# Performance work log

Hardware: AMD Instinct MI355X
Metric: run time of the kernel (lower is better)

Reference implementation:

```python
import jax, jax.numpy as jnp
import numpy as np

N_NODES = 65536
N_PER = 1024      # nodes per graph
NUM_GRAPHS = 64
N_EDGES = 1048576
IN_DIM = 192
PE_DIM = 64
HIDDEN = 256
LATENT = 128
POOL_RATIO = 0.5
K_PER = int(np.ceil(POOL_RATIO * N_PER))  # 512 kept per graph


def setup_inputs() -> dict:
    key = jax.random.key(0)
    ks = jax.random.split(key, 12)
    x_raw = jax.random.normal(ks[0], (N_NODES, IN_DIM), dtype=jnp.float32)
    sincos_pe = jax.random.normal(ks[1], (N_NODES, PE_DIM), dtype=jnp.float32)
    edge_index = jax.random.randint(ks[2], (2, N_EDGES), 0, N_NODES, dtype=jnp.int64)
    batch = (jnp.arange(N_NODES, dtype=jnp.int64) // N_PER)
    eps = jax.random.normal(ks[3], (N_NODES, LATENT), dtype=jnp.float32)
    # learned parameters (GCNConv: Linear no-bias weight + separate bias; TopKPooling weight)
    def glorot(k, shape):
        lim = float(np.sqrt(6.0 / (shape[0] + shape[1])))
        return jax.random.uniform(k, shape, jnp.float32, -lim, lim)
    W1 = glorot(ks[4], (IN_DIM + PE_DIM, HIDDEN))
    b1 = jnp.zeros((HIDDEN,), jnp.float32)
    Wmu = glorot(ks[5], (HIDDEN, LATENT))
    bmu = jnp.zeros((LATENT,), jnp.float32)
    Wlv = glorot(ks[6], (HIDDEN, LATENT))
    blv = jnp.zeros((LATENT,), jnp.float32)
    w_pool = jax.random.uniform(ks[7], (LATENT,), jnp.float32, -1.0, 1.0) / np.sqrt(LATENT)
    return {"x_raw": x_raw, "sincos_pe": sincos_pe, "edge_index": edge_index,
            "batch": batch, "eps": eps, "W1": W1, "b1": b1, "Wmu": Wmu,
            "bmu": bmu, "Wlv": Wlv, "blv": blv, "w_pool": w_pool}


def _gcn_conv(x, W, b, src, dst, n):
    # PyG GCNConv: x' = D^{-1/2}(A+I)D^{-1/2} (x W) + b, self-loops already in src/dst
    h = x @ W                                   # [N, out]
    deg = jnp.zeros((n,), h.dtype).at[dst].add(1.0)
    dinv = jax.lax.rsqrt(deg)                   # deg >= 1 thanks to self-loops
    norm = dinv[src] * dinv[dst]                # [E+N]
    msg = norm[:, None] * h[src]                # gather (irregular)
    return jax.ops.segment_sum(msg, dst, num_segments=n) + b


def reference(x_raw, sincos_pe, edge_index, batch, eps, W1, b1, Wmu, bmu, Wlv, blv, w_pool):
    n = x_raw.shape[0]
    loops = jnp.arange(n, dtype=edge_index.dtype)
    src = jnp.concatenate([edge_index[0], loops])
    dst = jnp.concatenate([edge_index[1], loops])

    x_in = jnp.concatenate([x_raw, sincos_pe], axis=-1)
    h = jax.nn.relu(_gcn_conv(x_in, W1, b1, src, dst, n))
    mu = _gcn_conv(h, Wmu, bmu, src, dst, n)
    logvar = _gcn_conv(h, Wlv, blv, src, dst, n)
    z = mu + eps * jnp.exp(0.5 * logvar)

    # TopKPooling: score = tanh((z . w)/||w||); keep top ratio per graph
    score = jnp.tanh((z @ w_pool) / jnp.linalg.norm(w_pool))   # [N]
    s2 = score.reshape(NUM_GRAPHS, N_PER)
    _, idx = jax.lax.top_k(s2, K_PER)                           # descending per graph
    perm = (idx + (jnp.arange(NUM_GRAPHS) * N_PER)[:, None]).reshape(-1)
    z_pool = z[perm] * score[perm][:, None]
    mu_pool = mu[perm]
    logvar_pool = logvar[perm]
    batch_pool = batch[perm]
    return z_pool, mu_pool, logvar_pool, batch_pool, perm
```

## Files before the change

### kernel.cpp

```cpp
#include <hip/hip_runtime.h>
#include <hip/hip_fp16.h>
#include <math.h>

#define NN      65536
#define NE      1048576
#define NPER    1024
#define NGRAPH  64
#define KPER    512
#define IND     192
#define PED     64
#define HID     256
#define LAT     128

#define OFF_CNT     0u
#define OFF_ROWPTR  65536u
#define OFF_CUR     132096u
#define OFF_DINV    198656u
#define OFF_EPK     264192u
#define OFF_INVWN   2361344u
#define OFF_KEEP    2361360u
#define OFF_SCORE   2395136u
#define OFF_WT1     2460672u
#define OFF_WT2     2493440u
#define OFF_T0B     2526208u
#define OFF_HB      6720512u
#define OFF_MUB     10914816u
#define OFF_LVB     15109120u

#define OUT_MU      4194304
#define OUT_LV      8388608
#define OUT_BATCH   12582912
#define OUT_PERM    12615680

typedef __attribute__((ext_vector_type(8))) short short8;
typedef __attribute__((ext_vector_type(4))) float floatx4;

__device__ __forceinline__ unsigned short f2bf(float f) {
    unsigned int u = __float_as_uint(f);
    u += 0x7FFFu + ((u >> 16) & 1u);
    return (unsigned short)(u >> 16);
}
__device__ __forceinline__ float bf2f(unsigned short u) {
    return __uint_as_float(((unsigned int)u) << 16);
}
__device__ __forceinline__ unsigned char f2e5(float f) {
    unsigned short u = __half_as_ushort(__float2half(f));
    u += (unsigned short)(0x7Fu + ((u >> 8) & 1u));
    return (unsigned char)(u >> 8);
}
__device__ __forceinline__ float e52f(unsigned char c) {
    return __half2float(__ushort_as_half((unsigned short)((unsigned short)c << 8)));
}
__device__ __forceinline__ __half2 e5lo(unsigned int u) {
    return __builtin_bit_cast(__half2, __builtin_amdgcn_perm(u, 0u, 0x05000400u));
}
__device__ __forceinline__ __half2 e5hi(unsigned int u) {
    return __builtin_bit_cast(__half2, __builtin_amdgcn_perm(u, 0u, 0x07000600u));
}

__global__ __launch_bounds__(256) void k_count(const int* __restrict__ ei, int* __restrict__ cnt) {
    int e = blockIdx.x * 256 + threadIdx.x;
    atomicAdd(&cnt[ei[NE + e]], 1);
}

__global__ __launch_bounds__(1024) void k_scan(const int* __restrict__ cnt, int* __restrict__ rp,
                                               float* __restrict__ dinv) {
    __shared__ int part[1024];
    const int t = threadIdx.x;
    const int base = t * 64;
    int loc[64];
#pragma unroll
    for (int i = 0; i < 64; i += 4)
        *(int4*)&loc[i] = *(const int4*)(cnt + base + i);
    int s = 0;
#pragma unroll
    for (int i = 0; i < 64; ++i) s += loc[i];
    part[t] = s;
    __syncthreads();
    for (int d = 1; d < 1024; d <<= 1) {
        int v = (t >= d) ? part[t - d] : 0;
        __syncthreads();
        part[t] += v;
        __syncthreads();
    }
    int run = part[t] - s;
    int rpo[64];
    float dv[64];
#pragma unroll
    for (int i = 0; i < 64; ++i) {
        rpo[i] = run;
        run += loc[i];
        dv[i] = 1.0f / sqrtf((float)(loc[i] + 1));
    }
#pragma unroll
    for (int i = 0; i < 64; i += 4) {
        *(int4*)(rp + base + i) = *(int4*)&rpo[i];
        *(float4*)(dinv + base + i) = *(float4*)&dv[i];
    }
    if (t == 1023) rp[NN] = run;
}

__global__ __launch_bounds__(256) void k_scatter(const int* __restrict__ ei, const int* __restrict__ rp,
                                                 int* __restrict__ cur, const float* __restrict__ dinv,
                                                 int2* __restrict__ epk) {
    int e = blockIdx.x * 256 + threadIdx.x;
    int s = ei[e];
    int d = ei[NE + e];
    int pos = rp[d] + atomicAdd(&cur[d], 1);
    epk[pos] = make_int2(s, __float_as_int(dinv[s] * dinv[d]));
}

__global__ __launch_bounds__(128) void k_wnorm(const float* __restrict__ wp, float* __restrict__ invwn) {
    __shared__ float red[128];
    int t = threadIdx.x;
    float v = wp[t];
    red[t] = v * v;
    __syncthreads();
    for (int s = 64; s > 0; s >>= 1) {
        if (t < s) red[t] += red[t + s];
        __syncthreads();
    }
    if (t == 0) invwn[0] = 1.0f / sqrtf(red[0]);
}

__global__ __launch_bounds__(256) void k_prepw(const float* __restrict__ W1, const float* __restrict__ Wmu,
                                               const float* __restrict__ Wlv, unsigned short* __restrict__ wt1,
                                               unsigned short* __restrict__ wt2) {
    const int n = blockIdx.x, k = threadIdx.x;
    wt1[n * 256 + k] = f2bf(W1[k * 256 + n]);
    wt2[n * 256 + k] = f2bf((n < 128) ? Wmu[k * 128 + n] : Wlv[k * 128 + (n - 128)]);
}

template <int MODE>
__global__ __launch_bounds__(256, 2) void k_gemm(const float* __restrict__ A0f, const float* __restrict__ A1f,
                                                 const unsigned char* __restrict__ Ab,
                                                 const unsigned short* __restrict__ Wt,
                                                 unsigned char* __restrict__ Cb) {
    __shared__ unsigned short lds[12288];
    const int tid = threadIdx.x;
    const int w = __builtin_amdgcn_readfirstlane(tid >> 6);
    const int lane = tid & 63;
    const int l = lane & 15, q = lane >> 4;
    const int Rbase = blockIdx.x * 128;

    const int rs = tid >> 1;
    const int ch = tid & 1;
    const int stile = rs >> 4, sl = rs & 15, q0 = ch * 2;
    const int uA = (stile * 4 + q0) * 16 + sl;

    floatx4 acc[16][2];
#pragma unroll
    for (int nt = 0; nt < 16; ++nt) {
        acc[nt][0] = (floatx4)0.0f;
        acc[nt][1] = (floatx4)0.0f;
    }

    for (int ks = 0; ks < 8; ++ks) {
        unsigned short abuf[16];
        if (MODE == 0) {
            const float* p; int ld, col;
            const int k = ks * 32 + ch * 16;
            if (ks < 6) { p = A0f; ld = IND; col = k; }
            else        { p = A1f; ld = PED; col = k - IND; }
            const float* src = p + (size_t)(Rbase + rs) * ld + col;
#pragma unroll
            for (int j = 0; j < 16; j += 4) {
                const float4 t = *(const float4*)(src + j);
                abuf[j] = f2bf(t.x); abuf[j + 1] = f2bf(t.y);
                abuf[j + 2] = f2bf(t.z); abuf[j + 3] = f2bf(t.w);
            }
        } else {
            const unsigned char* src = Ab + (size_t)(Rbase + rs) * 256 + ks * 32 + ch * 16;
            uint4 pk = *(const uint4*)src;
#pragma unroll
            for (int j = 0; j < 16; ++j) {
                unsigned char c = ((const unsigned char*)&pk)[j];
                abuf[j] = (unsigned short)(__float_as_uint(e52f(c)) >> 16);
            }
        }
        *(uint4*)&lds[uA * 8]        = *(uint4*)&abuf[0];
        *(uint4*)&lds[(uA + 16) * 8] = *(uint4*)&abuf[8];
#pragma unroll
        for (int rep = 0; rep < 2; ++rep) {
            const int n = rep * 128 + rs;
            const unsigned short* src = Wt + (size_t)n * 256 + ks * 32 + ch * 16;
            const uint4 w0 = ((const uint4*)src)[0];
            const uint4 w1 = ((const uint4*)src)[1];
            const int uB = ((n >> 4) * 4 + q0) * 16 + (n & 15);
            *(uint4*)&lds[4096 + uB * 8]        = w0;
            *(uint4*)&lds[4096 + (uB + 16) * 8] = w1;
        }
        __syncthreads();
        const short8 a0 = *(const short8*)&lds[(((2 * w) * 4 + q) * 16 + l) * 8];
        const short8 a1 = *(const short8*)&lds[(((2 * w + 1) * 4 + q) * 16 + l) * 8];
#pragma unroll
        for (int nt = 0; nt < 16; ++nt) {
            const short8 b = *(const short8*)&lds[4096 + ((nt * 4 + q) * 16 + l) * 8];
            acc[nt][0] = __builtin_amdgcn_mfma_f32_16x16x32_bf16(a0, b, acc[nt][0], 0, 0, 0);
            acc[nt][1] = __builtin_amdgcn_mfma_f32_16x16x32_bf16(a1, b, acc[nt][1], 0, 0, 0);
        }
        __syncthreads();
    }

#pragma unroll
    for (int m = 0; m < 2; ++m) {
        const int mt = 2 * w + m;
#pragma unroll
        for (int nt = 0; nt < 16; ++nt) {
            const floatx4 v = acc[nt][m];
            size_t base = (size_t)(Rbase + mt * 16 + q * 4) * 256 + nt * 16 + l;
            Cb[base]       = f2e5(v[0]);
            Cb[base + 256] = f2e5(v[1]);
            Cb[base + 512] = f2e5(v[2]);
            Cb[base + 768] = f2e5(v[3]);
        }
    }
}

template <int PHASE>
__global__ __launch_bounds__(256) void k_agg(const unsigned char* __restrict__ tb, const int* __restrict__ rp,
                                             const int2* __restrict__ epk, const float* __restrict__ dinv,
                                             const float* __restrict__ bias0, const float* __restrict__ bias1,
                                             const float* __restrict__ eps, const float* __restrict__ wp,
                                             const float* __restrict__ invwn, unsigned char* __restrict__ hb,
                                             unsigned short* __restrict__ mub, unsigned short* __restrict__ lvb,
                                             float* __restrict__ score) {
    const int wv = __builtin_amdgcn_readfirstlane(threadIdx.x >> 6);
    const int lane = threadIdx.x & 63;
    const int node = blockIdx.x * 4 + wv;
    const int c0 = lane * 4;
    const float di = dinv[node];

    const unsigned int vs = *(const unsigned int*)(tb + ((size_t)node << 8) + c0);
    const __half2 ws2 = __float2half2_rn(di * di);
    __half2 a01 = __hmul2(ws2, e5lo(vs));
    __half2 a23 = __hmul2(ws2, e5hi(vs));
    __half2 b01 = __float2half2_rn(0.0f);
    __half2 b23 = __float2half2_rn(0.0f);

    const int beg = rp[node], end = rp[node + 1];
    int p = beg;
    if (p + 4 <= end) {
        int2 e0 = epk[p], e1 = epk[p + 1], e2 = epk[p + 2], e3 = epk[p + 3];
        for (;;) {
            const int2 f0 = epk[p + 4], f1 = epk[p + 5], f2 = epk[p + 6], f3 = epk[p + 7];
            const int r0 = __builtin_amdgcn_readfirstlane(e0.x);
            const int r1 = __builtin_amdgcn_readfirstlane(e1.x);
            const int r2 = __builtin_amdgcn_readfirstlane(e2.x);
            const int r3 = __builtin_amdgcn_readfirstlane(e3.x);
            const unsigned int v0 = *(const unsigned int*)(tb + ((size_t)r0 << 8) + c0);
            const unsigned int v1 = *(const unsigned int*)(tb + ((size_t)r1 << 8) + c0);
            const unsigned int v2 = *(const unsigned int*)(tb + ((size_t)r2 << 8) + c0);
            const unsigned int v3 = *(const unsigned int*)(tb + ((size_t)r3 << 8) + c0);
            const __half2 w0 = __float2half2_rn(__int_as_float(e0.y));
            const __half2 w1 = __float2half2_rn(__int_as_float(e1.y));
            const __half2 w2 = __float2half2_rn(__int_as_float(e2.y));
            const __half2 w3 = __float2half2_rn(__int_as_float(e3.y));
            a01 = __hfma2(w0, e5lo(v0), a01); a23 = __hfma2(w0, e5hi(v0), a23);
            b01 = __hfma2(w1, e5lo(v1), b01); b23 = __hfma2(w1, e5hi(v1), b23);
            a01 = __hfma2(w2, e5lo(v2), a01); a23 = __hfma2(w2, e5hi(v2), a23);
            b01 = __hfma2(w3, e5lo(v3), b01); b23 = __hfma2(w3, e5hi(v3), b23);
            p += 4;
            if (p + 4 > end) break;
            e0 = f0; e1 = f1; e2 = f2; e3 = f3;
        }
    }
    for (; p < end; ++p) {
        const int2 e = epk[p];
        const int r = __builtin_amdgcn_readfirstlane(e.x);
        const unsigned int v = *(const unsigned int*)(tb + ((size_t)r << 8) + c0);
        const __half2 w2 = __float2half2_rn(__int_as_float(e.y));
        a01 = __hfma2(w2, e5lo(v), a01);
        a23 = __hfma2(w2, e5hi(v), a23);
    }
    a01 = __hadd2(a01, b01);
    a23 = __hadd2(a23, b23);
    const float2 flo = __half22float2(a01);
    const float2 fhi = __half22float2(a23);
    float4 acc = make_float4(flo.x, flo.y, fhi.x, fhi.y);

    if (PHASE == 0) {
        const float4 bb = *(const float4*)(bias0 + c0);
        uchar4 r;
        r.x = f2e5(fmaxf(acc.x + bb.x, 0.0f));
        r.y = f2e5(fmaxf(acc.y + bb.y, 0.0f));
        r.z = f2e5(fmaxf(acc.z + bb.z, 0.0f));
        r.w = f2e5(fmaxf(acc.w + bb.w, 0.0f));
        *(uchar4*)(hb + ((size_t)node << 8) + c0) = r;
    } else {
        const int cb = (lane & 31) * 4;
        const float* bias = (lane < 32) ? bias0 : bias1;
        const float4 bb = *(const float4*)(bias + cb);
        acc.x += bb.x; acc.y += bb.y; acc.z += bb.z; acc.w += bb.w;
        unsigned short* dst = (lane < 32) ? mub : lvb;
        ushort4 st;
        st.x = f2bf(acc.x); st.y = f2bf(acc.y); st.z = f2bf(acc.z); st.w = f2bf(acc.w);
        *(ushort4*)(dst + (size_t)node * 128 + cb) = st;
        float4 l4;
        l4.x = __shfl(acc.x, lane | 32, 64);
        l4.y = __shfl(acc.y, lane | 32, 64);
        l4.z = __shfl(acc.z, lane | 32, 64);
        l4.w = __shfl(acc.w, lane | 32, 64);
        float partial = 0.0f;
        if (lane < 32) {
            const float4 e4 = *(const float4*)(eps + (size_t)node * 128 + cb);
            const float4 w4 = *(const float4*)(wp + cb);
            float zx = fmaf(e4.x, expf(0.5f * l4.x), acc.x);
            float zy = fmaf(e4.y, expf(0.5f * l4.y), acc.y);
            float zz = fmaf(e4.z, expf(0.5f * l4.z), acc.z);
            float zw = fmaf(e4.w, expf(0.5f * l4.w), acc.w);
            partial = zx * w4.x + zy * w4.y + zz * w4.z + zw * w4.w;
        }
        for (int off = 16; off > 0; off >>= 1) partial += __shfl_xor(partial, off, 64);
        if (lane == 0) score[node] = tanhf(partial * invwn[0]);
    }
}

__global__ __launch_bounds__(512) void k_topk(const float* __restrict__ score, const int* __restrict__ batch,
                                              int* __restrict__ keep, float* __restrict__ out) {
    __shared__ float sk[1024];
    __shared__ int si[1024];
    const int g = blockIdx.x, t = threadIdx.x;
    for (int i = t; i < 1024; i += 512) {
        sk[i] = score[g * 1024 + i];
        si[i] = i;
    }
    __syncthreads();
    for (int k = 2; k <= 1024; k <<= 1) {
        for (int j = k >> 1; j > 0; j >>= 1) {
            for (int base = 0; base < 1024; base += 512) {
                int i = base + t;
                int ixj = i ^ j;
                if (ixj > i) {
                    float a = sk[i], b = sk[ixj];
                    int ia = si[i], ib = si[ixj];
                    bool before = (a > b) || (a == b && ia < ib);
                    bool up = ((i & k) == 0);
                    bool sw = up ? (!before) : before;
                    if (sw) {
                        sk[i] = b; si[i] = ib;
                        sk[ixj] = a; si[ixj] = ia;
                    }
                }
            }
            __syncthreads();
        }
    }
    if (t < KPER) {
        int node = g * 1024 + si[t];
        keep[g * KPER + t] = node;
        out[OUT_BATCH + g * KPER + t] = (float)batch[node];
        out[OUT_PERM + g * KPER + t] = (float)node;
    }
}

__global__ __launch_bounds__(128) void k_gather(const int* __restrict__ keep,
                                                const unsigned short* __restrict__ mub,
                                                const unsigned short* __restrict__ lvb,
                                                const float* __restrict__ eps,
                                                const float* __restrict__ score, float* __restrict__ out) {
    const int kidx = blockIdx.x;
    const int c = threadIdx.x;
    const int node = keep[kidx];
    const float m = bf2f(mub[(size_t)node * 128 + c]);
    const float l = bf2f(lvb[(size_t)node * 128 + c]);
    const float e = eps[(size_t)node * 128 + c];
    const float z = fmaf(e, expf(0.5f * l), m);
    const float s = score[node];
    out[(size_t)kidx * 128 + c] = z * s;
    out[OUT_MU + (size_t)kidx * 128 + c] = m;
    out[OUT_LV + (size_t)kidx * 128 + c] = l;
}

extern "C" void kernel_launch(void* const* d_in, const int* in_sizes, int n_in,
                              void* d_out, int out_size, void* d_ws, size_t ws_size,
                              hipStream_t stream) {
    (void)in_sizes; (void)n_in; (void)out_size; (void)ws_size;
    const float* x_raw = (const float*)d_in[0];
    const float* pe    = (const float*)d_in[1];
    const int*   ei    = (const int*)d_in[2];
    const int*   batch = (const int*)d_in[3];
    const float* eps   = (const float*)d_in[4];
    const float* W1    = (const float*)d_in[5];
    const float* b1    = (const float*)d_in[6];
    const float* Wmu   = (const float*)d_in[7];
    const float* bmu   = (const float*)d_in[8];
    const float* Wlv   = (const float*)d_in[9];
    const float* blv   = (const float*)d_in[10];
    const float* wp    = (const float*)d_in[11];
    float* ws = (float*)d_ws;
    int*  iws = (int*)d_ws;
    int2* epk = (int2*)(iws + OFF_EPK);
    unsigned short* wt1 = (unsigned short*)(ws + OFF_WT1);
    unsigned short* wt2 = (unsigned short*)(ws + OFF_WT2);
    unsigned char*  t0b = (unsigned char*)(ws + OFF_T0B);
    unsigned char*  hb  = (unsigned char*)(ws + OFF_HB);
    unsigned short* mub = (unsigned short*)(ws + OFF_MUB);
    unsigned short* lvb = (unsigned short*)(ws + OFF_LVB);
    float* out = (float*)d_out;

    hipMemsetAsync(iws + OFF_CNT, 0, 65536 * 4, stream);
    hipMemsetAsync(iws + OFF_CUR, 0, 65536 * 4, stream);

    k_count<<<NE / 256, 256, 0, stream>>>(ei, iws + OFF_CNT);
    k_scan<<<1, 1024, 0, stream>>>(iws + OFF_CNT, iws + OFF_ROWPTR, ws + OFF_DINV);
    k_scatter<<<NE / 256, 256, 0, stream>>>(ei, iws + OFF_ROWPTR, iws + OFF_CUR, ws + OFF_DINV, epk);
    k_wnorm<<<1, 128, 0, stream>>>(wp, ws + OFF_INVWN);
    k_prepw<<<256, 256, 0, stream>>>(W1, Wmu, Wlv, wt1, wt2);

    k_gemm<0><<<NN / 128, 256, 0, stream>>>(x_raw, pe, nullptr, wt1, t0b);
    k_agg<0><<<NN / 4, 256, 0, stream>>>(t0b, iws + OFF_ROWPTR, epk, ws + OFF_DINV,
                                         b1, nullptr, nullptr, nullptr, nullptr,
                                         hb, nullptr, nullptr, nullptr);
    k_gemm<1><<<NN / 128, 256, 0, stream>>>(nullptr, nullptr, hb, wt2, t0b);
    k_agg<1><<<NN / 4, 256, 0, stream>>>(t0b, iws + OFF_ROWPTR, epk, ws + OFF_DINV,
                                         bmu, blv, eps, wp, ws + OFF_INVWN,
                                         nullptr, mub, lvb, ws + OFF_SCORE);
    k_topk<<<NGRAPH, 512, 0, stream>>>(ws + OFF_SCORE, batch, iws + OFF_KEEP, out);
    k_gather<<<NGRAPH * KPER, 128, 0, stream>>>(iws + OFF_KEEP, mub, lvb, eps,
                                                ws + OFF_SCORE, out);
}
```

Before: 450.0 us.

## Double-buffer GEMM LDS staging, store hidden as bf16, unroll aggregation by eight

The GEMM kernel now uses two LDS buffers. It stages the next K-slice while MFMAs consume the current one, which drops one barrier per iteration. Input conversion uses a cheaper packed bf16 rounding, and output uses the hardware packed bf8 convert when it is available. The hidden activation h is stored as bf16 instead of 8-bit e5m2, which removes per-byte decoding in the second GEMM but doubles its read and write traffic. The gather-aggregation loop is unrolled from 4 to 8 edges to keep more loads in flight, and the mu/logvar buffers are moved to reuse the now-dead h region of the workspace.

```diff
diff --git a/kernel.cpp b/kernel.cpp
--- a/kernel.cpp
+++ b/kernel.cpp
@@ -24,8 +24,8 @@
 #define OFF_WT2     2493440u
 #define OFF_T0B     2526208u
 #define OFF_HB      6720512u
-#define OFF_MUB     10914816u
-#define OFF_LVB     15109120u
+#define OFF_MUB     6720512u
+#define OFF_LVB     10914816u
 
 #define OUT_MU      4194304
 #define OUT_LV      8388608
@@ -43,13 +43,27 @@
 __device__ __forceinline__ float bf2f(unsigned short u) {
     return __uint_as_float(((unsigned int)u) << 16);
 }
+__device__ __forceinline__ unsigned int pack2bf(float x, float y) {
+    const unsigned int ux = __float_as_uint(x) + 0x8000u;
+    const unsigned int uy = __float_as_uint(y) + 0x8000u;
+    return __builtin_amdgcn_perm(uy, ux, 0x07060302u);
+}
 __device__ __forceinline__ unsigned char f2e5(float f) {
     unsigned short u = __half_as_ushort(__float2half(f));
     u += (unsigned short)(0x7Fu + ((u >> 8) & 1u));
     return (unsigned char)(u >> 8);
 }
-__device__ __forceinline__ float e52f(unsigned char c) {
-    return __half2float(__ushort_as_half((unsigned short)((unsigned short)c << 8)));
+__device__ __forceinline__ void store_bf8x4(unsigned char* base, float v0, float v1, float v2, float v3) {
+#if __has_builtin(__builtin_amdgcn_cvt_pk_bf8_f32)
+    const unsigned int r01 = (unsigned int)__builtin_amdgcn_cvt_pk_bf8_f32(v0, v1, 0, false);
+    const unsigned int r23 = (unsigned int)__builtin_amdgcn_cvt_pk_bf8_f32(v2, v3, 0, false);
+    base[0]   = (unsigned char)r01;
+    base[256] = (unsigned char)(r01 >> 8);
+    base[512] = (unsigned char)r23;
+    base[768] = (unsigned char)(r23 >> 8);
+#else
+    base[0] = f2e5(v0); base[256] = f2e5(v1); base[512] = f2e5(v2); base[768] = f2e5(v3);
+#endif
 }
 __device__ __forceinline__ __half2 e5lo(unsigned int u) {
     return __builtin_bit_cast(__half2, __builtin_amdgcn_perm(u, 0u, 0x05000400u));
@@ -133,10 +147,10 @@
 
 template <int MODE>
 __global__ __launch_bounds__(256, 2) void k_gemm(const float* __restrict__ A0f, const float* __restrict__ A1f,
-                                                 const unsigned char* __restrict__ Ab,
+                                                 const unsigned short* __restrict__ Ah,
                                                  const unsigned short* __restrict__ Wt,
                                                  unsigned char* __restrict__ Cb) {
-    __shared__ unsigned short lds[12288];
+    __shared__ unsigned short lds[2][12288];
     const int tid = threadIdx.x;
     const int w = __builtin_amdgcn_readfirstlane(tid >> 6);
     const int lane = tid & 63;
@@ -155,51 +169,54 @@
         acc[nt][1] = (floatx4)0.0f;
     }
 
-    for (int ks = 0; ks < 8; ++ks) {
-        unsigned short abuf[16];
+    auto stage = [&](int ks, int buf) {
         if (MODE == 0) {
             const float* p; int ld, col;
             const int k = ks * 32 + ch * 16;
             if (ks < 6) { p = A0f; ld = IND; col = k; }
             else        { p = A1f; ld = PED; col = k - IND; }
             const float* src = p + (size_t)(Rbase + rs) * ld + col;
+            unsigned int pk[8];
 #pragma unroll
             for (int j = 0; j < 16; j += 4) {
                 const float4 t = *(const float4*)(src + j);
-                abuf[j] = f2bf(t.x); abuf[j + 1] = f2bf(t.y);
-                abuf[j + 2] = f2bf(t.z); abuf[j + 3] = f2bf(t.w);
+                pk[j / 2]     = pack2bf(t.x, t.y);
+                pk[j / 2 + 1] = pack2bf(t.z, t.w);
             }
+            *(uint4*)&lds[buf][uA * 8]        = *(uint4*)&pk[0];
+            *(uint4*)&lds[buf][(uA + 16) * 8] = *(uint4*)&pk[4];
         } else {
-            const unsigned char* src = Ab + (size_t)(Rbase + rs) * 256 + ks * 32 + ch * 16;
-            uint4 pk = *(const uint4*)src;
-#pragma unroll
-            for (int j = 0; j < 16; ++j) {
-                unsigned char c = ((const unsigned char*)&pk)[j];
-                abuf[j] = (unsigned short)(__float_as_uint(e52f(c)) >> 16);
-            }
-        }
-        *(uint4*)&lds[uA * 8]        = *(uint4*)&abuf[0];
-        *(uint4*)&lds[(uA + 16) * 8] = *(uint4*)&abuf[8];
+            const unsigned short* src = Ah + (size_t)(Rbase + rs) * 256 + ks * 32 + ch * 16;
+            *(uint4*)&lds[buf][uA * 8]        = ((const uint4*)src)[0];
+            *(uint4*)&lds[buf][(uA + 16) * 8] = ((const uint4*)src)[1];
+        }
 #pragma unroll
         for (int rep = 0; rep < 2; ++rep) {
             const int n = rep * 128 + rs;
-            const unsigned short* src = Wt + (size_t)n * 256 + ks * 32 + ch * 16;
-            const uint4 w0 = ((const uint4*)src)[0];
-            const uint4 w1 = ((const uint4*)src)[1];
+            const unsigned short* srcB = Wt + (size_t)n * 256 + ks * 32 + ch * 16;
+            const uint4 w0 = ((const uint4*)srcB)[0];
+            const uint4 w1 = ((const uint4*)srcB)[1];
             const int uB = ((n >> 4) * 4 + q0) * 16 + (n & 15);
-            *(uint4*)&lds[4096 + uB * 8]        = w0;
-            *(uint4*)&lds[4096 + (uB + 16) * 8] = w1;
-        }
-        __syncthreads();
-        const short8 a0 = *(const short8*)&lds[(((2 * w) * 4 + q) * 16 + l) * 8];
-        const short8 a1 = *(const short8*)&lds[(((2 * w + 1) * 4 + q) * 16 + l) * 8];
+            *(uint4*)&lds[buf][4096 + uB * 8]        = w0;
+            *(uint4*)&lds[buf][4096 + (uB + 16) * 8] = w1;
+        }
+    };
+
+    stage(0, 0);
+    __syncthreads();
+#pragma unroll
+    for (int ks = 0; ks < 8; ++ks) {
+        const int cur = ks & 1;
+        if (ks < 7) stage(ks + 1, cur ^ 1);
+        const short8 a0 = *(const short8*)&lds[cur][(((2 * w) * 4 + q) * 16 + l) * 8];
+        const short8 a1 = *(const short8*)&lds[cur][(((2 * w + 1) * 4 + q) * 16 + l) * 8];
 #pragma unroll
         for (int nt = 0; nt < 16; ++nt) {
-            const short8 b = *(const short8*)&lds[4096 + ((nt * 4 + q) * 16 + l) * 8];
+            const short8 b = *(const short8*)&lds[cur][4096 + ((nt * 4 + q) * 16 + l) * 8];
             acc[nt][0] = __builtin_amdgcn_mfma_f32_16x16x32_bf16(a0, b, acc[nt][0], 0, 0, 0);
             acc[nt][1] = __builtin_amdgcn_mfma_f32_16x16x32_bf16(a1, b, acc[nt][1], 0, 0, 0);
         }
-        __syncthreads();
+        if (ks < 7) __syncthreads();
     }
 
 #pragma unroll
@@ -208,11 +225,8 @@
 #pragma unroll
         for (int nt = 0; nt < 16; ++nt) {
             const floatx4 v = acc[nt][m];
-            size_t base = (size_t)(Rbase + mt * 16 + q * 4) * 256 + nt * 16 + l;
-            Cb[base]       = f2e5(v[0]);
-            Cb[base + 256] = f2e5(v[1]);
-            Cb[base + 512] = f2e5(v[2]);
-            Cb[base + 768] = f2e5(v[3]);
+            unsigned char* base = Cb + (size_t)(Rbase + mt * 16 + q * 4) * 256 + nt * 16 + l;
+            store_bf8x4(base, v[0], v[1], v[2], v[3]);
         }
     }
 }
@@ -222,7 +236,7 @@
                                              const int2* __restrict__ epk, const float* __restrict__ dinv,
                                              const float* __restrict__ bias0, const float* __restrict__ bias1,
                                              const float* __restrict__ eps, const float* __restrict__ wp,
-                                             const float* __restrict__ invwn, unsigned char* __restrict__ hb,
+                                             const float* __restrict__ invwn, unsigned short* __restrict__ hb,
                                              unsigned short* __restrict__ mub, unsigned short* __restrict__ lvb,
                                              float* __restrict__ score) {
     const int wv = __builtin_amdgcn_readfirstlane(threadIdx.x >> 6);
@@ -230,8 +244,9 @@
     const int node = blockIdx.x * 4 + wv;
     const int c0 = lane * 4;
     const float di = dinv[node];
-
-    const unsigned int vs = *(const unsigned int*)(tb + ((size_t)node << 8) + c0);
+    const unsigned char* tbc = tb + c0;
+
+    const unsigned int vs = *(const unsigned int*)(tbc + ((size_t)node << 8));
     const __half2 ws2 = __float2half2_rn(di * di);
     __half2 a01 = __hmul2(ws2, e5lo(vs));
     __half2 a23 = __hmul2(ws2, e5hi(vs));
@@ -240,35 +255,61 @@
 
     const int beg = rp[node], end = rp[node + 1];
     int p = beg;
-    if (p + 4 <= end) {
-        int2 e0 = epk[p], e1 = epk[p + 1], e2 = epk[p + 2], e3 = epk[p + 3];
+    if (p + 8 <= end) {
+        int2 e0 = epk[p],     e1 = epk[p + 1], e2 = epk[p + 2], e3 = epk[p + 3];
+        int2 e4 = epk[p + 4], e5 = epk[p + 5], e6 = epk[p + 6], e7 = epk[p + 7];
         for (;;) {
-            const int2 f0 = epk[p + 4], f1 = epk[p + 5], f2 = epk[p + 6], f3 = epk[p + 7];
-            const int r0 = __builtin_amdgcn_readfirstlane(e0.x);
-            const int r1 = __builtin_amdgcn_readfirstlane(e1.x);
-            const int r2 = __builtin_amdgcn_readfirstlane(e2.x);
-            const int r3 = __builtin_amdgcn_readfirstlane(e3.x);
-            const unsigned int v0 = *(const unsigned int*)(tb + ((size_t)r0 << 8) + c0);
-            const unsigned int v1 = *(const unsigned int*)(tb + ((size_t)r1 << 8) + c0);
-            const unsigned int v2 = *(const unsigned int*)(tb + ((size_t)r2 << 8) + c0);
-            const unsigned int v3 = *(const unsigned int*)(tb + ((size_t)r3 << 8) + c0);
+            const int2 f0 = epk[p + 8],  f1 = epk[p + 9],  f2 = epk[p + 10], f3 = epk[p + 11];
+            const int2 f4 = epk[p + 12], f5 = epk[p + 13], f6 = epk[p + 14], f7 = epk[p + 15];
+            const unsigned int v0 = *(const unsigned int*)(tbc + ((size_t)__builtin_amdgcn_readfirstlane(e0.x) << 8));
+            const unsigned int v1 = *(const unsigned int*)(tbc + ((size_t)__builtin_amdgcn_readfirstlane(e1.x) << 8));
+            const unsigned int v2 = *(const unsigned int*)(tbc + ((size_t)__builtin_amdgcn_readfirstlane(e2.x) << 8));
+            const unsigned int v3 = *(const unsigned int*)(tbc + ((size_t)__builtin_amdgcn_readfirstlane(e3.x) << 8));
+            const unsigned int v4 = *(const unsigned int*)(tbc + ((size_t)__builtin_amdgcn_readfirstlane(e4.x) << 8));
+            const unsigned int v5 = *(const unsigned int*)(tbc + ((size_t)__builtin_amdgcn_readfirstlane(e5.x) << 8));
+            const unsigned int v6 = *(const unsigned int*)(tbc + ((size_t)__builtin_amdgcn_readfirstlane(e6.x) << 8));
+            const unsigned int v7 = *(const unsigned int*)(tbc + ((size_t)__builtin_amdgcn_readfirstlane(e7.x) << 8));
             const __half2 w0 = __float2half2_rn(__int_as_float(e0.y));
             const __half2 w1 = __float2half2_rn(__int_as_float(e1.y));
             const __half2 w2 = __float2half2_rn(__int_as_float(e2.y));
             const __half2 w3 = __float2half2_rn(__int_as_float(e3.y));
+            const __half2 w4 = __float2half2_rn(__int_as_float(e4.y));
+            const __half2 w5 = __float2half2_rn(__int_as_float(e5.y));
+            const __half2 w6 = __float2half2_rn(__int_as_float(e6.y));
+            const __half2 w7 = __float2half2_rn(__int_as_float(e7.y));
             a01 = __hfma2(w0, e5lo(v0), a01); a23 = __hfma2(w0, e5hi(v0), a23);
             b01 = __hfma2(w1, e5lo(v1), b01); b23 = __hfma2(w1, e5hi(v1), b23);
             a01 = __hfma2(w2, e5lo(v2), a01); a23 = __hfma2(w2, e5hi(v2), a23);
             b01 = __hfma2(w3, e5lo(v3), b01); b23 = __hfma2(w3, e5hi(v3), b23);
-            p += 4;
-            if (p + 4 > end) break;
+            a01 = __hfma2(w4, e5lo(v4), a01); a23 = __hfma2(w4, e5hi(v4), a23);
+            b01 = __hfma2(w5, e5lo(v5), b01); b23 = __hfma2(w5, e5hi(v5), b23);
+            a01 = __hfma2(w6, e5lo(v6), a01); a23 = __hfma2(w6, e5hi(v6), a23);
+            b01 = __hfma2(w7, e5lo(v7), b01); b23 = __hfma2(w7, e5hi(v7), b23);
+            p += 8;
+            if (p + 8 > end) break;
             e0 = f0; e1 = f1; e2 = f2; e3 = f3;
-        }
+            e4 = f4; e5 = f5; e6 = f6; e7 = f7;
+        }
+    }
+    if (p + 4 <= end) {
+        const int2 e0 = epk[p], e1 = epk[p + 1], e2 = epk[p + 2], e3 = epk[p + 3];
+        const unsigned int v0 = *(const unsigned int*)(tbc + ((size_t)__builtin_amdgcn_readfirstlane(e0.x) << 8));
+        const unsigned int v1 = *(const unsigned int*)(tbc + ((size_t)__builtin_amdgcn_readfirstlane(e1.x) << 8));
+        const unsigned int v2 = *(const unsigned int*)(tbc + ((size_t)__builtin_amdgcn_readfirstlane(e2.x) << 8));
+        const unsigned int v3 = *(const unsigned int*)(tbc + ((size_t)__builtin_amdgcn_readfirstlane(e3.x) << 8));
+        const __half2 w0 = __float2half2_rn(__int_as_float(e0.y));
+        const __half2 w1 = __float2half2_rn(__int_as_float(e1.y));
+        const __half2 w2 = __float2half2_rn(__int_as_float(e2.y));
+        const __half2 w3 = __float2half2_rn(__int_as_float(e3.y));
+        a01 = __hfma2(w0, e5lo(v0), a01); a23 = __hfma2(w0, e5hi(v0), a23);
+        b01 = __hfma2(w1, e5lo(v1), b01); b23 = __hfma2(w1, e5hi(v1), b23);
+        a01 = __hfma2(w2, e5lo(v2), a01); a23 = __hfma2(w2, e5hi(v2), a23);
+        b01 = __hfma2(w3, e5lo(v3), b01); b23 = __hfma2(w3, e5hi(v3), b23);
+        p += 4;
     }
     for (; p < end; ++p) {
         const int2 e = epk[p];
-        const int r = __builtin_amdgcn_readfirstlane(e.x);
-        const unsigned int v = *(const unsigned int*)(tb + ((size_t)r << 8) + c0);
+        const unsigned int v = *(const unsigned int*)(tbc + ((size_t)__builtin_amdgcn_readfirstlane(e.x) << 8));
         const __half2 w2 = __float2half2_rn(__int_as_float(e.y));
         a01 = __hfma2(w2, e5lo(v), a01);
         a23 = __hfma2(w2, e5hi(v), a23);
@@ -281,12 +322,12 @@
 
     if (PHASE == 0) {
         const float4 bb = *(const float4*)(bias0 + c0);
-        uchar4 r;
-        r.x = f2e5(fmaxf(acc.x + bb.x, 0.0f));
-        r.y = f2e5(fmaxf(acc.y + bb.y, 0.0f));
-        r.z = f2e5(fmaxf(acc.z + bb.z, 0.0f));
-        r.w = f2e5(fmaxf(acc.w + bb.w, 0.0f));
-        *(uchar4*)(hb + ((size_t)node << 8) + c0) = r;
+        ushort4 r;
+        r.x = f2bf(fmaxf(acc.x + bb.x, 0.0f));
+        r.y = f2bf(fmaxf(acc.y + bb.y, 0.0f));
+        r.z = f2bf(fmaxf(acc.z + bb.z, 0.0f));
+        r.w = f2bf(fmaxf(acc.w + bb.w, 0.0f));
+        *(ushort4*)(hb + ((size_t)node << 8) + c0) = r;
     } else {
         const int cb = (lane & 31) * 4;
         const float* bias = (lane < 32) ? bias0 : bias1;
@@ -391,12 +432,12 @@
     float* ws = (float*)d_ws;
     int*  iws = (int*)d_ws;
     int2* epk = (int2*)(iws + OFF_EPK);
-    unsigned short* wt1 = (unsigned short*)(ws + OFF_WT1);
-    unsigned short* wt2 = (unsigned short*)(ws + OFF_WT2);
-    unsigned char*  t0b = (unsigned char*)(ws + OFF_T0B);
-    unsigned char*  hb  = (unsigned char*)(ws + OFF_HB);
-    unsigned short* mub = (unsigned short*)(ws + OFF_MUB);
-    unsigned short* lvb = (unsigned short*)(ws + OFF_LVB);
+    unsigned short* wt1  = (unsigned short*)(ws + OFF_WT1);
+    unsigned short* wt2  = (unsigned short*)(ws + OFF_WT2);
+    unsigned char*  t0b  = (unsigned char*)(ws + OFF_T0B);
+    unsigned short* hb16 = (unsigned short*)(ws + OFF_HB);
+    unsigned short* mub  = (unsigned short*)(ws + OFF_MUB);
+    unsigned short* lvb  = (unsigned short*)(ws + OFF_LVB);
     float* out = (float*)d_out;
 
     hipMemsetAsync(iws + OFF_CNT, 0, 65536 * 4, stream);
@@ -411,8 +452,8 @@
     k_gemm<0><<<NN / 128, 256, 0, stream>>>(x_raw, pe, nullptr, wt1, t0b);
     k_agg<0><<<NN / 4, 256, 0, stream>>>(t0b, iws + OFF_ROWPTR, epk, ws + OFF_DINV,
                                          b1, nullptr, nullptr, nullptr, nullptr,
-                                         hb, nullptr, nullptr, nullptr);
-    k_gemm<1><<<NN / 128, 256, 0, stream>>>(nullptr, nullptr, hb, wt2, t0b);
+                                         hb16, nullptr, nullptr, nullptr);
+    k_gemm<1><<<NN / 128, 256, 0, stream>>>(nullptr, nullptr, hb16, wt2, t0b);
     k_agg<1><<<NN / 4, 256, 0, stream>>>(t0b, iws + OFF_ROWPTR, epk, ws + OFF_DINV,
                                          bmu, blv, eps, wp, ws + OFF_INVWN,
                                          nullptr, mub, lvb, ws + OFF_SCORE);
```

Result: no change. 442.4 us (-1.7%).
